# Optimization experiments

Measured on AMD Instinct MI355X. Metric: run time of the kernel, lower is better.

Reference implementation:

```python
import jax, jax.numpy as jnp
import numpy as np

B, C, H, W = 32, 1024, 48, 24
P = 3            # num_parts
IC = C // 8      # inter_channels for position attention
PH = H // P      # part height


def setup_inputs() -> dict:
    key = jax.random.key(0)
    ks = jax.random.split(key, 16)
    s = 0.02
    return {
        "x": jax.random.normal(ks[0], (B, C, H, W), jnp.float32),
        "modality": jax.random.randint(ks[1], (B,), 0, 2),
        # per-part 1x1 conv weights (stacked over parts)
        "Wq": jax.random.normal(ks[2], (P, IC, C), jnp.float32) * s,
        "bq": jnp.zeros((P, IC), jnp.float32),
        "Wk": jax.random.normal(ks[3], (P, IC, C), jnp.float32) * s,
        "bk": jnp.zeros((P, IC), jnp.float32),
        "Wv": jax.random.normal(ks[4], (P, C, C), jnp.float32) * s,
        "bv": jnp.zeros((P, C), jnp.float32),
        # gamma residual scales (torch inits to 0; random so output differs from x)
        "gamma_pa": jax.random.normal(ks[5], (P,), jnp.float32) * 0.1,
        "gamma_ca": jax.random.normal(ks[6], (P,), jnp.float32) * 0.1,
        # modality gate: Linear(1,64) -> ReLU -> Linear(64,P) -> Sigmoid
        "gW1": jax.random.normal(ks[7], (64, 1), jnp.float32) * 0.01,
        "gb1": jnp.zeros((64,), jnp.float32),
        "gW2": jax.random.normal(ks[8], (P, 64), jnp.float32) * 0.01,
        "gb2": jnp.zeros((P,), jnp.float32),
    }


def _part_dual_attn(part, Wq, bq, Wk, bk, Wv, bv, g_pa, g_ca):
    # part: [B, C, ph, W]
    b, c, ph, w = part.shape
    n = ph * w
    xf = part.reshape(b, c, n)  # [B,C,N]
    # --- Position attention (PAM) ---
    q = jnp.einsum('oc,bcn->bno', Wq, xf) + bq            # [B,N,IC]
    k = jnp.einsum('oc,bcn->bon', Wk, xf) + bk[:, None]   # [B,IC,N]
    attn = jax.nn.softmax(jnp.einsum('bno,bom->bnm', q, k), axis=-1)  # [B,N,N]
    v = jnp.einsum('oc,bcn->bon', Wv, xf) + bv[:, None]   # [B,C,N]
    pa = jnp.einsum('bcn,bmn->bcm', v, attn).reshape(part.shape)
    pa = g_pa * pa + part
    # --- Channel attention (CAM) with max-shifted softmax ---
    e = jnp.einsum('bcn,bdn->bcd', xf, xf)                # [B,C,C]
    e = jnp.max(e, axis=-1, keepdims=True) - e
    ca_attn = jax.nn.softmax(e, axis=-1)
    ca = jnp.einsum('bcd,bdn->bcn', ca_attn, xf).reshape(part.shape)
    ca = g_ca * ca + part
    return pa + ca


def reference(x, modality, Wq, bq, Wk, bk, Wv, bv, gamma_pa, gamma_ca, gW1, gb1, gW2, gb2):
    b = x.shape[0]
    # modality gate -> per-sample per-part blend weights [B,P]
    m = modality.astype(jnp.float32)[:, None]
    h = jax.nn.relu(m @ gW1.T + gb1)
    w_gate = jax.nn.sigmoid(h @ gW2.T + gb2)              # [B,P]
    # split into P horizontal parts: [P,B,C,ph,W]
    parts = x.reshape(b, C, P, PH, W).transpose(2, 0, 1, 3, 4)
    part_outs = jax.vmap(_part_dual_attn)(parts, Wq, bq, Wk, bk, Wv, bv, gamma_pa, gamma_ca)
    wp = w_gate.T[:, :, None, None, None]                 # [P,B,1,1,1]
    blended = parts * (1.0 - wp) + part_outs * wp         # [P,B,C,ph,W]
    return blended.transpose(1, 2, 0, 3, 4).reshape(b, C, H, W)
```

## Files before the change

### kernel.cpp

```cpp
#include <hip/hip_runtime.h>
#include <hip/hip_bf16.h>
#include <cstdint>

constexpr int kB  = 32;
constexpr int kC  = 1024;
constexpr int kH  = 48;
constexpr int kW  = 24;
constexpr int kP  = 3;
constexpr int kPH = 16;
constexpr int kN  = kPH * kW;
constexpr int kHW = kH * kW;
constexpr int64_t kCHW = (int64_t)kC * kHW;

typedef __attribute__((ext_vector_type(8))) short short8b;
typedef __attribute__((ext_vector_type(4))) float f32x4;

__device__ __forceinline__ void gl_lds16(const void* g, void* l) {
    __builtin_amdgcn_global_load_lds(
        (const __attribute__((address_space(1))) void*)g,
        (__attribute__((address_space(3))) void*)l, 16, 0, 0);
}

__device__ __forceinline__ void swz_block(int& bx, int& by, int& bz) {
    const int gx = gridDim.x, gy = gridDim.y, gz = gridDim.z;
    if ((gz & 7) == 0) {
        const int tpp = gx * gy;
        const int L   = (blockIdx.z * gy + blockIdx.y) * gx + blockIdx.x;
        const int xcd = L & 7;
        const int idx = L >> 3;
        const int ppx = gz >> 3;
        const int pairL = idx / tpp;
        const int tile  = idx - pairL * tpp;
        bz = xcd * ppx + pairL;
        by = tile / gx;
        bx = tile - by * gx;
    } else {
        bx = blockIdx.x; by = blockIdx.y; bz = blockIdx.z;
    }
}

#define WAIT8()       asm volatile("s_waitcnt vmcnt(8)" ::: "memory")
#define WAIT4()       asm volatile("s_waitcnt vmcnt(4)" ::: "memory")
#define WAIT0()       asm volatile("s_waitcnt vmcnt(0)" ::: "memory")
#define RAW_BARRIER() asm volatile("s_barrier" ::: "memory")
#define SFENCE()      __builtin_amdgcn_sched_barrier(0)

__global__ void gate_kernel(const int* __restrict__ modality,
                            const float* __restrict__ gW1, const float* __restrict__ gb1,
                            const float* __restrict__ gW2, const float* __restrict__ gb2,
                            const float* __restrict__ gpa, const float* __restrict__ gca,
                            const float* __restrict__ bq, const float* __restrict__ bk,
                            float* __restrict__ wg, float* __restrict__ cpa,
                            float* __restrict__ cca, float* __restrict__ bqk)
{
    const int t = threadIdx.x;
    if (t < 768) {
        const int p = t >> 8, o = t & 255;
        bqk[t] = (o < 128) ? bq[p * 128 + o] : bk[p * 128 + (o - 128)];
    }
    if (t < kB * kP) {
        const int b = t / kP, p = t % kP;
        const float m = (float)modality[b];
        float acc = gb2[p];
        #pragma unroll
        for (int j = 0; j < 64; ++j) {
            float h = fmaxf(fmaf(m, gW1[j], gb1[j]), 0.0f);
            acc = fmaf(gW2[p * 64 + j], h, acc);
        }
        const float w = 1.0f / (1.0f + __expf(-acc));
        wg[t]  = w;
        cpa[t] = w * gpa[p];
        cca[t] = w * gca[p];
    }
}

__global__ __launch_bounds__(256)
void wcast_kernel(const float* __restrict__ Wq, const float* __restrict__ Wk,
                  const float* __restrict__ Wv,
                  __hip_bfloat16* __restrict__ Wqkb, __hip_bfloat16* __restrict__ Wvb)
{
    const int64_t i = (int64_t)blockIdx.x * 256 + threadIdx.x;
    if (i < 196608) {
        const int64_t e = i * 4;
        const int p = (int)(e / 262144);
        const int rem = (int)(e % 262144);
        const int o = rem / 1024, c = rem % 1024;
        const float* s = (o < 128) ? (Wq + (int64_t)p * 131072 + (int64_t)o * 1024 + c)
                                   : (Wk + (int64_t)p * 131072 + (int64_t)(o - 128) * 1024 + c);
        float4 v = *(const float4*)s;
        __hip_bfloat16* d = Wqkb + e;
        d[0] = __float2bfloat16(v.x); d[1] = __float2bfloat16(v.y);
        d[2] = __float2bfloat16(v.z); d[3] = __float2bfloat16(v.w);
    } else if (i < 196608 + 786432) {
        const int64_t e = (i - 196608) * 4;
        float4 v = *(const float4*)(Wv + e);
        __hip_bfloat16* d = Wvb + e;
        d[0] = __float2bfloat16(v.x); d[1] = __float2bfloat16(v.y);
        d[2] = __float2bfloat16(v.z); d[3] = __float2bfloat16(v.w);
    }
}

__global__ void zeroz_kernel(float* __restrict__ Z)
{
    Z[(int64_t)blockIdx.x * 1024 + threadIdx.x] = 0.0f;
}

__global__ __launch_bounds__(256)
void cast_tr_kernel(const float* __restrict__ x,
                    __hip_bfloat16* __restrict__ xfb,
                    __hip_bfloat16* __restrict__ xfT)
{
    int bx, by, bz;
    swz_block(bx, by, bz);
    const int j = bz;
    const int bb = j / kP, pp = j % kP;
    const float* src = x + (int64_t)bb * kCHW + pp * kN;
    const int c0 = bx * 32, n0 = by * 32;
    __shared__ float tile[32][33];
    const int tx = threadIdx.x & 31, ty = threadIdx.x >> 5;
    #pragma unroll
    for (int r = 0; r < 4; ++r) {
        const int cl = ty * 4 + r;
        const int c = c0 + cl;
        float v = src[(int64_t)c * kHW + n0 + tx];
        xfb[(int64_t)j * 393216 + (int64_t)c * kN + n0 + tx] = __float2bfloat16(v);
        tile[tx][cl] = v;
    }
    __syncthreads();
    #pragma unroll
    for (int r = 0; r < 4; ++r) {
        const int nl = ty * 4 + r;
        xfT[(int64_t)j * 393216 + (int64_t)(n0 + nl) * kC + c0 + tx] =
            __float2bfloat16(tile[nl][tx]);
    }
}

template<int BIAS>
__global__ __launch_bounds__(256, 2)
void mm_kernel(const __hip_bfloat16* __restrict__ A0, int64_t aSB, int64_t aSP, int lda,
               const __hip_bfloat16* __restrict__ B0, int64_t bSB, int64_t bSP, int ldb,
               __hip_bfloat16* __restrict__ C0, int64_t cSB, int64_t cSP, int ldc,
               const float* __restrict__ bias0, int biasSP, int K)
{
    __shared__ char lds[65536];

    int bx, by, bz;
    swz_block(bx, by, bz);
    const int j = bz, bb = j / kP, pp = j % kP;
    const char* Ab = (const char*)(A0 + (int64_t)bb * aSB + (int64_t)pp * aSP);
    const char* Bb = (const char*)(B0 + (int64_t)bb * bSB + (int64_t)pp * bSP);
    const int m0 = bx * 128, n0 = by * 128;
    const int t = threadIdx.x, lane = t & 63, wv = t >> 6;
    const int wm = (wv & 1) * 64, wn = (wv >> 1) * 64;
    const size_t ldab = (size_t)lda * 2, ldbb = (size_t)ldb * 2;

    const int rr   = wv * 8 + (lane >> 3);
    const int gsrc = ((lane & 7) ^ (lane >> 3)) * 16;
    const int lrow = (wv * 8 + (lane >> 3)) * 128 + (lane & 7) * 16;

    auto STAGE = [&](int buf, int k0) {
        const char* Asrc = Ab + (size_t)(m0 + rr) * ldab + (size_t)k0 * 2 + gsrc;
        const char* Bsrc = Bb + (size_t)(n0 + rr) * ldbb + (size_t)k0 * 2 + gsrc;
        char* As = lds + buf * 32768;
        char* Bs = As + 16384;
        #pragma unroll
        for (int i = 0; i < 4; ++i) {
            gl_lds16(Asrc + (size_t)i * 32 * ldab, As + i * 4096 + lrow);
            gl_lds16(Bsrc + (size_t)i * 32 * ldbb, Bs + i * 4096 + lrow);
        }
    };

    f32x4 acc[4][4];
    #pragma unroll
    for (int a = 0; a < 4; ++a)
        #pragma unroll
        for (int b = 0; b < 4; ++b) acc[a][b] = (f32x4){0.f, 0.f, 0.f, 0.f};

    const int nk = K >> 6;
    STAGE(0, 0);
    int cur = 0;
    for (int k = 0; k < nk; ++k) {
        if (k + 1 < nk) { STAGE(cur ^ 1, (k + 1) << 6); WAIT8(); }
        else            { WAIT0(); }
        SFENCE();
        RAW_BARRIER();
        const char* As = lds + cur * 32768;
        const char* Bs = As + 16384;
        #pragma unroll
        for (int kk = 0; kk < 2; ++kk) {
            const int gpos = ((kk * 4 + (lane >> 4)) ^ (lane & 7)) * 16;
            short8b af[4], bf[4];
            #pragma unroll
            for (int f = 0; f < 4; ++f) {
                af[f] = *(const short8b*)(As + (wm + f * 16 + (lane & 15)) * 128 + gpos);
                bf[f] = *(const short8b*)(Bs + (wn + f * 16 + (lane & 15)) * 128 + gpos);
            }
            #pragma unroll
            for (int fm = 0; fm < 4; ++fm)
                #pragma unroll
                for (int fn = 0; fn < 4; ++fn)
                    acc[fm][fn] = __builtin_amdgcn_mfma_f32_16x16x32_bf16(
                        af[fm], bf[fn], acc[fm][fn], 0, 0, 0);
        }
        RAW_BARRIER();
        cur ^= 1;
    }

    __hip_bfloat16* Cm = C0 + (int64_t)bb * cSB + (int64_t)pp * cSP;
    #pragma unroll
    for (int fn = 0; fn < 4; ++fn) {
        const int col = n0 + wn + fn * 16 + (lane & 15);
        const float cb = (BIAS == 2) ? bias0[pp * biasSP + col] : 0.0f;
        #pragma unroll
        for (int fm = 0; fm < 4; ++fm)
            #pragma unroll
            for (int jr = 0; jr < 4; ++jr) {
                const int row = m0 + wm + fm * 16 + (lane >> 4) * 4 + jr;
                Cm[(int64_t)row * ldc + col] = __float2bfloat16(acc[fm][fn][jr] + cb);
            }
    }
}

__global__ __launch_bounds__(256, 2)
void ecam_kernel(const __hip_bfloat16* __restrict__ xfb,
                 __hip_bfloat16* __restrict__ eb,
                 float* __restrict__ Z)
{
    __shared__ char lds[65536];

    int bx, by, bz;
    swz_block(bx, by, bz);
    const int j = bz;
    int bi = 0;
    while ((bi + 1) * (bi + 2) / 2 <= bx) ++bi;
    const int bj = bx - bi * (bi + 1) / 2;
    const char* Ab = (const char*)(xfb + (int64_t)j * 393216);
    const int m0 = bi * 128, n0 = bj * 128;
    const int t = threadIdx.x, lane = t & 63, wv = t >> 6;
    const int wm = (wv & 1) * 64, wn = (wv >> 1) * 64;
    constexpr size_t ldab = 768;

    const int rr   = wv * 8 + (lane >> 3);
    const int gsrc = ((lane & 7) ^ (lane >> 3)) * 16;
    const int lrow = (wv * 8 + (lane >> 3)) * 128 + (lane & 7) * 16;

    auto STAGE = [&](int buf, int k0) {
        const char* Asrc = Ab + (size_t)(m0 + rr) * ldab + (size_t)k0 * 2 + gsrc;
        const char* Bsrc = Ab + (size_t)(n0 + rr) * ldab + (size_t)k0 * 2 + gsrc;
        char* As = lds + buf * 32768;
        char* Bs = As + 16384;
        #pragma unroll
        for (int i = 0; i < 4; ++i) {
            gl_lds16(Asrc + (size_t)i * 32 * ldab, As + i * 4096 + lrow);
            gl_lds16(Bsrc + (size_t)i * 32 * ldab, Bs + i * 4096 + lrow);
        }
    };

    f32x4 acc[4][4];
    #pragma unroll
    for (int a = 0; a < 4; ++a)
        #pragma unroll
        for (int b = 0; b < 4; ++b) acc[a][b] = (f32x4){0.f, 0.f, 0.f, 0.f};

    STAGE(0, 0);
    int cur = 0;
    for (int k = 0; k < 6; ++k) {
        if (k + 1 < 6) { STAGE(cur ^ 1, (k + 1) << 6); WAIT8(); }
        else           { WAIT0(); }
        SFENCE();
        RAW_BARRIER();
        const char* As = lds + cur * 32768;
        const char* Bs = As + 16384;
        #pragma unroll
        for (int kk = 0; kk < 2; ++kk) {
            const int gpos = ((kk * 4 + (lane >> 4)) ^ (lane & 7)) * 16;
            short8b af[4], bf[4];
            #pragma unroll
            for (int f = 0; f < 4; ++f) {
                af[f] = *(const short8b*)(As + (wm + f * 16 + (lane & 15)) * 128 + gpos);
                bf[f] = *(const short8b*)(Bs + (wn + f * 16 + (lane & 15)) * 128 + gpos);
            }
            #pragma unroll
            for (int fm = 0; fm < 4; ++fm)
                #pragma unroll
                for (int fn = 0; fn < 4; ++fn)
                    acc[fm][fn] = __builtin_amdgcn_mfma_f32_16x16x32_bf16(
                        af[fm], bf[fn], acc[fm][fn], 0, 0, 0);
        }
        RAW_BARRIER();
        cur ^= 1;
    }

    #pragma unroll
    for (int fm = 0; fm < 4; ++fm)
        #pragma unroll
        for (int fn = 0; fn < 4; ++fn)
            #pragma unroll
            for (int jr = 0; jr < 4; ++jr)
                acc[fm][fn][jr] = __expf(-60.f - acc[fm][fn][jr]);

    __hip_bfloat16* Cm = eb + (int64_t)j * 1048576;
    float* Zp = Z + (int64_t)j * 1024;

    #pragma unroll
    for (int fm = 0; fm < 4; ++fm)
        #pragma unroll
        for (int jr = 0; jr < 4; ++jr) {
            const int row = m0 + wm + fm * 16 + (lane >> 4) * 4 + jr;
            float v = 0.f;
            #pragma unroll
            for (int fn = 0; fn < 4; ++fn) {
                const int col = n0 + wn + fn * 16 + (lane & 15);
                Cm[(int64_t)row * 1024 + col] = __float2bfloat16(acc[fm][fn][jr]);
                v += acc[fm][fn][jr];
            }
            v += __shfl_xor(v, 1);
            v += __shfl_xor(v, 2);
            v += __shfl_xor(v, 4);
            v += __shfl_xor(v, 8);
            if ((lane & 15) == 0) atomicAdd(Zp + row, v);
        }

    if (bi != bj) {
        #pragma unroll
        for (int fn = 0; fn < 4; ++fn) {
            const int col = n0 + wn + fn * 16 + (lane & 15);
            float v2 = 0.f;
            #pragma unroll
            for (int fm = 0; fm < 4; ++fm) {
                const int row0 = m0 + wm + fm * 16 + (lane >> 4) * 4;
                __hip_bfloat16 h0 = __float2bfloat16(acc[fm][fn][0]);
                __hip_bfloat16 h1 = __float2bfloat16(acc[fm][fn][1]);
                __hip_bfloat16 h2 = __float2bfloat16(acc[fm][fn][2]);
                __hip_bfloat16 h3 = __float2bfloat16(acc[fm][fn][3]);
                ushort4 w4;
                w4.x = *(ushort*)&h0; w4.y = *(ushort*)&h1;
                w4.z = *(ushort*)&h2; w4.w = *(ushort*)&h3;
                *(ushort4*)((ushort*)Cm + (int64_t)col * 1024 + row0) = w4;
                v2 += (acc[fm][fn][0] + acc[fm][fn][1]) +
                      (acc[fm][fn][2] + acc[fm][fn][3]);
            }
            v2 += __shfl_xor(v2, 16);
            v2 += __shfl_xor(v2, 32);
            if ((lane >> 4) == 0) atomicAdd(Zp + col, v2);
        }
    }
}

__global__ __launch_bounds__(256, 3)
void ep_cam_kernel(const __hip_bfloat16* __restrict__ Wvb,
                   const __hip_bfloat16* __restrict__ yTb,
                   const __hip_bfloat16* __restrict__ eb,
                   const __hip_bfloat16* __restrict__ xfT,
                   const float* __restrict__ Z,
                   const float* __restrict__ x,
                   float* __restrict__ out,
                   const float* __restrict__ wg,
                   const float* __restrict__ cpa,
                   const float* __restrict__ cca,
                   const float* __restrict__ bv)
{
    __shared__ char lds[49152];

    int bx, by, bz;
    swz_block(bx, by, bz);
    const int j = bz, bb = j / kP, pp = j % kP;
    const int m0 = bx * 128, n0 = by * 128;
    const int t = threadIdx.x, lane = t & 63, wv = t >> 6;
    const int wm = (wv & 1) * 64, wn = (wv >> 1) * 64;

    const int rr4  = lane >> 2;
    const int gsrc = (((lane & 3) ^ ((lane >> 3) & 3)) * 16);
    const int ldst = lane * 16;

    const char* AbW = (const char*)(Wvb + (int64_t)pp * 1048576);
    const char* AbE = (const char*)(eb  + (int64_t)j  * 1048576);
    const char* BbY = (const char*)(yTb + (int64_t)j * 393216);
    const char* BbX = (const char*)(xfT + (int64_t)j * 393216);

    auto STAGE = [&](int buf, int g) {
        const char* A = (g < 32) ? AbE : AbW;
        const char* B = (g < 32) ? BbX : BbY;
        const size_t k0b = (size_t)(g & 31) * 64;
        const char* Asrc = A + (size_t)(m0 + wv * 32 + rr4) * 2048 + k0b + gsrc;
        const char* Bsrc = B + (size_t)(n0 + wv * 32 + rr4) * 2048 + k0b + gsrc;
        char* As = lds + buf * 16384;
        char* Bs = As + 8192;
        #pragma unroll
        for (int i = 0; i < 2; ++i) {
            gl_lds16(Asrc + (size_t)i * 16 * 2048, As + wv * 2048 + i * 1024 + ldst);
            gl_lds16(Bsrc + (size_t)i * 16 * 2048, Bs + wv * 2048 + i * 1024 + ldst);
        }
    };

    const float cfc = cca[j];
    const float* Zp = Z + (int64_t)j * 1024;
    float zsc[4][4];
    #pragma unroll
    for (int fm = 0; fm < 4; ++fm)
        #pragma unroll
        for (int jr = 0; jr < 4; ++jr) {
            const int row = m0 + wm + fm * 16 + (lane >> 4) * 4 + jr;
            zsc[fm][jr] = cfc / Zp[row];
        }

    f32x4 acc[4][4];
    #pragma unroll
    for (int a = 0; a < 4; ++a)
        #pragma unroll
        for (int b = 0; b < 4; ++b) acc[a][b] = (f32x4){0.f, 0.f, 0.f, 0.f};

    const int gpos = ((lane >> 4) ^ ((lane >> 1) & 3)) * 16;

    STAGE(0, 0);
    STAGE(1, 1);
    int cur = 0;
    for (int g = 0; g < 64; ++g) {
        if (g < 62) {
            int nb = cur + 2; if (nb >= 3) nb -= 3;
            STAGE(nb, g + 2);
            WAIT8();
        } else if (g == 62) { WAIT4(); }
        else                { WAIT0(); }
        SFENCE();
        RAW_BARRIER();
        if (g == 32) {
            #pragma unroll
            for (int fm = 0; fm < 4; ++fm)
                #pragma unroll
                for (int jr = 0; jr < 4; ++jr) {
                    const float zs = zsc[fm][jr];
                    #pragma unroll
                    for (int fn = 0; fn < 4; ++fn) acc[fm][fn][jr] *= zs;
                }
        }
        const char* As = lds + cur * 16384;
        const char* Bs = As + 8192;
        short8b af[4], bf[4];
        #pragma unroll
        for (int f = 0; f < 4; ++f) {
            af[f] = *(const short8b*)(As + (wm + f * 16 + (lane & 15)) * 64 + gpos);
            bf[f] = *(const short8b*)(Bs + (wn + f * 16 + (lane & 15)) * 64 + gpos);
        }
        #pragma unroll
        for (int fm = 0; fm < 4; ++fm)
            #pragma unroll
            for (int fn = 0; fn < 4; ++fn)
                acc[fm][fn] = __builtin_amdgcn_mfma_f32_16x16x32_bf16(
                    af[fm], bf[fn], acc[fm][fn], 0, 0, 0);
        RAW_BARRIER();
        if (++cur == 3) cur = 0;
    }

    const float gsc = 1.0f + wg[j];
    const float cfp = cpa[j];
    const float* Xm = x   + (int64_t)bb * kCHW + pp * kN;
    float*       Om = out + (int64_t)bb * kCHW + pp * kN;
    #pragma unroll
    for (int fm = 0; fm < 4; ++fm)
        #pragma unroll
        for (int jr = 0; jr < 4; ++jr) {
            const int row = m0 + wm + fm * 16 + (lane >> 4) * 4 + jr;
            const float rb = cfp * bv[pp * 1024 + row];
            #pragma unroll
            for (int fn = 0; fn < 4; ++fn) {
                const int col = n0 + wn + fn * 16 + (lane & 15);
                const int64_t off = (int64_t)row * kHW + col;
                Om[off] = fmaf(gsc, Xm[off], acc[fm][fn][jr] + rb);
            }
        }
}

__global__ __launch_bounds__(64) void sm_pam(__hip_bfloat16* __restrict__ buf,
                                             const float* __restrict__ scale,
                                             int chPairs)
{
    const int L = blockIdx.x;
    int pair, row;
    if ((chPairs & 7) == 0) {
        const int xcd = L & 7, idx = L >> 3;
        pair = xcd * (chPairs >> 3) + idx / kN;
        row  = idx % kN;
    } else { pair = L / kN; row = L % kN; }
    __hip_bfloat16* rp = buf + (int64_t)pair * (kN * kN) + (int64_t)row * kN;
    const int t = threadIdx.x;
    float v[6];
    float mx = -3.402823466e38f;
    #pragma unroll
    for (int r = 0; r < 6; ++r) {
        v[r] = __bfloat162float(rp[t + 64 * r]);
        mx = fmaxf(mx, v[r]);
    }
    #pragma unroll
    for (int off = 32; off > 0; off >>= 1) mx = fmaxf(mx, __shfl_xor(mx, off));
    float s = 0.0f;
    #pragma unroll
    for (int r = 0; r < 6; ++r) { v[r] = __expf(v[r] - mx); s += v[r]; }
    #pragma unroll
    for (int off = 32; off > 0; off >>= 1) s += __shfl_xor(s, off);
    const float inv = scale[pair] / s;
    #pragma unroll
    for (int r = 0; r < 6; ++r) rp[t + 64 * r] = __float2bfloat16(v[r] * inv);
}

extern "C" void kernel_launch(void* const* d_in, const int* in_sizes, int n_in,
                              void* d_out, int out_size, void* d_ws, size_t ws_size,
                              hipStream_t stream)
{
    const float* x   = (const float*)d_in[0];
    const int*   mod = (const int*)d_in[1];
    const float* Wq  = (const float*)d_in[2];
    const float* bq  = (const float*)d_in[3];
    const float* Wk  = (const float*)d_in[4];
    const float* bk  = (const float*)d_in[5];
    const float* Wv  = (const float*)d_in[6];
    const float* bv  = (const float*)d_in[7];
    const float* gpa = (const float*)d_in[8];
    const float* gca = (const float*)d_in[9];
    const float* gW1 = (const float*)d_in[10];
    const float* gb1 = (const float*)d_in[11];
    const float* gW2 = (const float*)d_in[12];
    const float* gb2 = (const float*)d_in[13];
    float* out = (float*)d_out;

    const int chList[6] = {96, 48, 24, 12, 6, 3};
    int CH = 3;
    for (int i = 0; i < 6; ++i) {
        size_t need = 7868544ull + (size_t)chList[i] * 4952064ull;
        if (need <= ws_size) { CH = chList[i]; break; }
    }
    const int NCHUNK = 96 / CH;

    char* ws = (char*)d_ws;
    __hip_bfloat16* Wqkb = (__hip_bfloat16*)(ws + 0);
    __hip_bfloat16* Wvb  = (__hip_bfloat16*)(ws + 1572864);
    float* bqk = (float*)(ws + 7864320);
    float* wg  = (float*)(ws + 7867392);
    float* cpa = (float*)(ws + 7867776);
    float* cca = (float*)(ws + 7868160);
    __hip_bfloat16* xfT   = (__hip_bfloat16*)(ws + 7868544);
    __hip_bfloat16* xfb   = xfT   + (int64_t)CH * 393216;
    __hip_bfloat16* qkT   = xfb   + (int64_t)CH * 393216;
    __hip_bfloat16* attnb = qkT   + (int64_t)CH * 98304;
    __hip_bfloat16* yTb   = attnb + (int64_t)CH * 147456;
    __hip_bfloat16* eb    = yTb   + (int64_t)CH * 393216;
    float*          Zbuf  = (float*)(eb + (int64_t)CH * 1048576);

    gate_kernel<<<1, 768, 0, stream>>>(mod, gW1, gb1, gW2, gb2, gpa, gca, bq, bk,
                                       wg, cpa, cca, bqk);
    wcast_kernel<<<3840, 256, 0, stream>>>(Wq, Wk, Wv, Wqkb, Wvb);

    for (int ch = 0; ch < NCHUNK; ++ch) {
        const int pair0 = ch * CH;
        const int b0 = pair0 / kP;
        const float* xc   = x   + (int64_t)b0 * kCHW;
        float*       outc = out + (int64_t)b0 * kCHW;

        cast_tr_kernel<<<dim3(32, 12, CH), 256, 0, stream>>>(xc, xfb, xfT);
        zeroz_kernel<<<CH, 1024, 0, stream>>>(Zbuf);

        mm_kernel<2><<<dim3(3, 2, CH), 256, 0, stream>>>(
            xfT, 3 * 393216, 393216, 1024,
            Wqkb, 0, 262144, 1024,
            qkT, 3 * 98304, 98304, 256,
            bqk, 256, 1024);
        mm_kernel<0><<<dim3(3, 3, CH), 256, 0, stream>>>(
            qkT, 3 * 98304, 98304, 256,
            qkT + 128, 3 * 98304, 98304, 256,
            attnb, 3 * 147456, 147456, 384,
            nullptr, 0, 128);
        sm_pam<<<CH * kN, 64, 0, stream>>>(attnb, cpa + pair0, CH);
        mm_kernel<0><<<dim3(3, 8, CH), 256, 0, stream>>>(
            attnb, 3 * 147456, 147456, 384,
            xfb, 3 * 393216, 393216, 384,
            yTb, 3 * 393216, 393216, 1024,
            nullptr, 0, 384);
        ecam_kernel<<<dim3(36, 1, CH), 256, 0, stream>>>(xfb, eb, Zbuf);
        ep_cam_kernel<<<dim3(8, 3, CH), 256, 0, stream>>>(
            Wvb, yTb, eb, xfT, Zbuf, xc, outc,
            wg + pair0, cpa + pair0, cca + pair0, bv);
    }
}
```

Before: 559.9 us.

## Enlarge ep_cam tile to 256x128 with 8 waves and interleaved LDS/MFMA phases

The CAM/value epilogue GEMM now uses 512-thread blocks, each computing a 256x128 output tile. K steps widen to 64 elements, so LDS reuse per global byte goes up and the main loop runs fewer iterations. The triple-buffered LDS grows to 144KB of dynamic shared memory with an 8-way XOR swizzle. Each K step is split into four barrier-separated sub-phases that interleave LDS fragment loads with MFMA bursts, and `s_setprio` raises wave priority during MFMA issue. In exchange, occupancy drops to one large block per CU, there are more barriers per step, and the kernel relies on a large dynamic LDS allocation being allowed.

Result: no change. 565.4 us (+1.0%).

```diff
diff --git a/kernel.cpp b/kernel.cpp
--- a/kernel.cpp
+++ b/kernel.cpp
@@ -40,8 +40,9 @@
 }
 
 #define WAIT8()       asm volatile("s_waitcnt vmcnt(8)" ::: "memory")
-#define WAIT4()       asm volatile("s_waitcnt vmcnt(4)" ::: "memory")
+#define WAIT6()       asm volatile("s_waitcnt vmcnt(6)" ::: "memory")
 #define WAIT0()       asm volatile("s_waitcnt vmcnt(0)" ::: "memory")
+#define LGKM0()       asm volatile("s_waitcnt lgkmcnt(0)" ::: "memory")
 #define RAW_BARRIER() asm volatile("s_barrier" ::: "memory")
 #define SFENCE()      __builtin_amdgcn_sched_barrier(0)
 
@@ -347,7 +348,7 @@
     }
 }
 
-__global__ __launch_bounds__(256, 3)
+__global__ __launch_bounds__(512, 2)
 void ep_cam_kernel(const __hip_bfloat16* __restrict__ Wvb,
                    const __hip_bfloat16* __restrict__ yTb,
                    const __hip_bfloat16* __restrict__ eb,
@@ -360,18 +361,18 @@
                    const float* __restrict__ cca,
                    const float* __restrict__ bv)
 {
-    __shared__ char lds[49152];
+    extern __shared__ char lds[];
 
     int bx, by, bz;
     swz_block(bx, by, bz);
     const int j = bz, bb = j / kP, pp = j % kP;
-    const int m0 = bx * 128, n0 = by * 128;
+    const int m0 = bx * 256, n0 = by * 128;
     const int t = threadIdx.x, lane = t & 63, wv = t >> 6;
-    const int wm = (wv & 1) * 64, wn = (wv >> 1) * 64;
-
-    const int rr4  = lane >> 2;
-    const int gsrc = (((lane & 3) ^ ((lane >> 3) & 3)) * 16);
-    const int ldst = lane * 16;
+    const int wm = (wv & 3) * 64, wn = (wv >> 2) * 64;
+
+    const int rr   = wv * 8 + (lane >> 3);
+    const int gsrc = ((lane & 7) ^ ((lane >> 3) & 7)) * 16;
+    const int ldst = wv * 1024 + lane * 16;
 
     const char* AbW = (const char*)(Wvb + (int64_t)pp * 1048576);
     const char* AbE = (const char*)(eb  + (int64_t)j  * 1048576);
@@ -379,18 +380,19 @@
     const char* BbX = (const char*)(xfT + (int64_t)j * 393216);
 
     auto STAGE = [&](int buf, int g) {
-        const char* A = (g < 32) ? AbE : AbW;
-        const char* B = (g < 32) ? BbX : BbY;
-        const size_t k0b = (size_t)(g & 31) * 64;
-        const char* Asrc = A + (size_t)(m0 + wv * 32 + rr4) * 2048 + k0b + gsrc;
-        const char* Bsrc = B + (size_t)(n0 + wv * 32 + rr4) * 2048 + k0b + gsrc;
-        char* As = lds + buf * 16384;
-        char* Bs = As + 8192;
-        #pragma unroll
-        for (int i = 0; i < 2; ++i) {
-            gl_lds16(Asrc + (size_t)i * 16 * 2048, As + wv * 2048 + i * 1024 + ldst);
-            gl_lds16(Bsrc + (size_t)i * 16 * 2048, Bs + wv * 2048 + i * 1024 + ldst);
-        }
+        const char* A = (g < 16) ? AbE : AbW;
+        const char* B = (g < 16) ? BbX : BbY;
+        const size_t k0b = (size_t)(g & 15) * 128;
+        const char* Asrc = A + (size_t)(m0 + rr) * 2048 + k0b + gsrc;
+        const char* Bsrc = B + (size_t)(n0 + rr) * 2048 + k0b + gsrc;
+        char* As = lds + (size_t)buf * 49152;
+        char* Bs = As + 32768;
+        #pragma unroll
+        for (int i = 0; i < 4; ++i)
+            gl_lds16(Asrc + (size_t)i * 64 * 2048, As + i * 8192 + ldst);
+        #pragma unroll
+        for (int i = 0; i < 2; ++i)
+            gl_lds16(Bsrc + (size_t)i * 64 * 2048, Bs + i * 8192 + ldst);
     };
 
     const float cfc = cca[j];
@@ -410,21 +412,33 @@
         #pragma unroll
         for (int b = 0; b < 4; ++b) acc[a][b] = (f32x4){0.f, 0.f, 0.f, 0.f};
 
-    const int gpos = ((lane >> 4) ^ ((lane >> 1) & 3)) * 16;
+    const int ro  = (lane & 15) * 128;
+    const int gp0 = (((lane >> 4)    ) ^ (lane & 7)) * 16;
+    const int gp1 = (((lane >> 4) + 4) ^ (lane & 7)) * 16;
+
+#define LDA_(FM, GP) (*(const short8b*)(As + (wm + (FM) * 16) * 128 + ro + (GP)))
+#define LDB_(FN, GP) (*(const short8b*)(Bs + (wn + (FN) * 16) * 128 + ro + (GP)))
+#define MM4(FM, AF)                                                              \
+    acc[FM][0] = __builtin_amdgcn_mfma_f32_16x16x32_bf16(AF, b0, acc[FM][0], 0, 0, 0); \
+    acc[FM][1] = __builtin_amdgcn_mfma_f32_16x16x32_bf16(AF, b1, acc[FM][1], 0, 0, 0); \
+    acc[FM][2] = __builtin_amdgcn_mfma_f32_16x16x32_bf16(AF, b2, acc[FM][2], 0, 0, 0); \
+    acc[FM][3] = __builtin_amdgcn_mfma_f32_16x16x32_bf16(AF, b3, acc[FM][3], 0, 0, 0);
 
     STAGE(0, 0);
     STAGE(1, 1);
+    WAIT6();
+    SFENCE();
+    RAW_BARRIER();
+
     int cur = 0;
-    for (int g = 0; g < 64; ++g) {
-        if (g < 62) {
-            int nb = cur + 2; if (nb >= 3) nb -= 3;
-            STAGE(nb, g + 2);
-            WAIT8();
-        } else if (g == 62) { WAIT4(); }
-        else                { WAIT0(); }
-        SFENCE();
-        RAW_BARRIER();
-        if (g == 32) {
+    #pragma unroll 1
+    for (int s = 0; s < 32; ++s) {
+        int nb = cur - 1; if (nb < 0) nb = 2;
+        const char* As = lds + (size_t)cur * 49152;
+        const char* Bs = As + 32768;
+        short8b a0, a1, a2, a3, b0, b1, b2, b3;
+
+        if (s == 16) {
             #pragma unroll
             for (int fm = 0; fm < 4; ++fm)
                 #pragma unroll
@@ -434,23 +448,49 @@
                     for (int fn = 0; fn < 4; ++fn) acc[fm][fn][jr] *= zs;
                 }
         }
-        const char* As = lds + cur * 16384;
-        const char* Bs = As + 8192;
-        short8b af[4], bf[4];
-        #pragma unroll
-        for (int f = 0; f < 4; ++f) {
-            af[f] = *(const short8b*)(As + (wm + f * 16 + (lane & 15)) * 64 + gpos);
-            bf[f] = *(const short8b*)(Bs + (wn + f * 16 + (lane & 15)) * 64 + gpos);
-        }
-        #pragma unroll
-        for (int fm = 0; fm < 4; ++fm)
-            #pragma unroll
-            for (int fn = 0; fn < 4; ++fn)
-                acc[fm][fn] = __builtin_amdgcn_mfma_f32_16x16x32_bf16(
-                    af[fm], bf[fn], acc[fm][fn], 0, 0, 0);
-        RAW_BARRIER();
-        if (++cur == 3) cur = 0;
-    }
+
+        a0 = LDA_(0, gp0); a1 = LDA_(1, gp0);
+        b0 = LDB_(0, gp0); b1 = LDB_(1, gp0); b2 = LDB_(2, gp0); b3 = LDB_(3, gp0);
+        if (s < 30) STAGE(nb, s + 2);
+        RAW_BARRIER();
+        LGKM0(); SFENCE();
+        __builtin_amdgcn_s_setprio(1);
+        MM4(0, a0); MM4(1, a1);
+        __builtin_amdgcn_s_setprio(0);
+        RAW_BARRIER();
+
+        a2 = LDA_(2, gp0); a3 = LDA_(3, gp0);
+        RAW_BARRIER();
+        LGKM0(); SFENCE();
+        __builtin_amdgcn_s_setprio(1);
+        MM4(2, a2); MM4(3, a3);
+        __builtin_amdgcn_s_setprio(0);
+        RAW_BARRIER();
+
+        a0 = LDA_(0, gp1); a1 = LDA_(1, gp1);
+        b0 = LDB_(0, gp1); b1 = LDB_(1, gp1); b2 = LDB_(2, gp1); b3 = LDB_(3, gp1);
+        RAW_BARRIER();
+        LGKM0(); SFENCE();
+        __builtin_amdgcn_s_setprio(1);
+        MM4(0, a0); MM4(1, a1);
+        __builtin_amdgcn_s_setprio(0);
+        RAW_BARRIER();
+
+        a2 = LDA_(2, gp1); a3 = LDA_(3, gp1);
+        RAW_BARRIER();
+        LGKM0(); SFENCE();
+        __builtin_amdgcn_s_setprio(1);
+        MM4(2, a2); MM4(3, a3);
+        __builtin_amdgcn_s_setprio(0);
+        if (s < 30) { WAIT6(); } else { WAIT0(); }
+        SFENCE();
+        RAW_BARRIER();
+
+        ++cur; if (cur == 3) cur = 0;
+    }
+#undef LDA_
+#undef LDB_
+#undef MM4
 
     const float gsc = 1.0f + wg[j];
     const float cfp = cpa[j];
@@ -576,7 +616,7 @@
             yTb, 3 * 393216, 393216, 1024,
             nullptr, 0, 384);
         ecam_kernel<<<dim3(36, 1, CH), 256, 0, stream>>>(xfb, eb, Zbuf);
-        ep_cam_kernel<<<dim3(8, 3, CH), 256, 0, stream>>>(
+        ep_cam_kernel<<<dim3(4, 3, CH), 512, 147456, stream>>>(
             Wvb, yTb, eb, xfT, Zbuf, xc, outc,
             wg + pair0, cpa + pair0, cca + pair0, bv);
     }
```

## Enlarge ep_cam tile to 512x128 with 8 waves and dynamic LDS

Applied to the files above, without the earlier changes.

Retiles the final fused CAM/value GEMM epilogue kernel from 128x128 tiles with 4 waves to 512x128 tiles with 8 waves. Each wave now computes a 128x64 sub-tile in two halves, and the triple-buffered LDS stages grow to 40 KB each (120 KB dynamic shared memory). The vmcnt waits are adjusted to match five loads per thread per stage. The aim is more reuse of the B operand and fewer redundant global loads. In exchange, occupancy drops to one block per CU, register pressure rises with 128 accumulator floats per thread, and the grid shrinks fourfold.

Result: slower. 605.3 us (+8.1%).

```diff
diff --git a/kernel.cpp b/kernel.cpp
--- a/kernel.cpp
+++ b/kernel.cpp
@@ -39,8 +39,9 @@
     }
 }
 
+#define WAIT10()      asm volatile("s_waitcnt vmcnt(10)" ::: "memory")
 #define WAIT8()       asm volatile("s_waitcnt vmcnt(8)" ::: "memory")
-#define WAIT4()       asm volatile("s_waitcnt vmcnt(4)" ::: "memory")
+#define WAIT5()       asm volatile("s_waitcnt vmcnt(5)" ::: "memory")
 #define WAIT0()       asm volatile("s_waitcnt vmcnt(0)" ::: "memory")
 #define RAW_BARRIER() asm volatile("s_barrier" ::: "memory")
 #define SFENCE()      __builtin_amdgcn_sched_barrier(0)
@@ -347,7 +348,7 @@
     }
 }
 
-__global__ __launch_bounds__(256, 3)
+__global__ __launch_bounds__(512, 1)
 void ep_cam_kernel(const __hip_bfloat16* __restrict__ Wvb,
                    const __hip_bfloat16* __restrict__ yTb,
                    const __hip_bfloat16* __restrict__ eb,
@@ -360,18 +361,18 @@
                    const float* __restrict__ cca,
                    const float* __restrict__ bv)
 {
-    __shared__ char lds[49152];
+    extern __shared__ char lds[];
 
     int bx, by, bz;
     swz_block(bx, by, bz);
     const int j = bz, bb = j / kP, pp = j % kP;
-    const int m0 = bx * 128, n0 = by * 128;
+    const int m0 = bx * 512, n0 = by * 128;
     const int t = threadIdx.x, lane = t & 63, wv = t >> 6;
-    const int wm = (wv & 1) * 64, wn = (wv >> 1) * 64;
-
-    const int rr4  = lane >> 2;
-    const int gsrc = (((lane & 3) ^ ((lane >> 3) & 3)) * 16);
-    const int ldst = lane * 16;
+    const int wm = (wv & 3) * 128, wn = (wv >> 2) * 64;
+
+    const int rr   = t >> 2;
+    const int gsrc = ((t & 3) ^ ((t >> 3) & 3)) * 16;
+    const int ldst = wv * 1024 + lane * 16;
 
     const char* AbW = (const char*)(Wvb + (int64_t)pp * 1048576);
     const char* AbE = (const char*)(eb  + (int64_t)j  * 1048576);
@@ -382,31 +383,30 @@
         const char* A = (g < 32) ? AbE : AbW;
         const char* B = (g < 32) ? BbX : BbY;
         const size_t k0b = (size_t)(g & 31) * 64;
-        const char* Asrc = A + (size_t)(m0 + wv * 32 + rr4) * 2048 + k0b + gsrc;
-        const char* Bsrc = B + (size_t)(n0 + wv * 32 + rr4) * 2048 + k0b + gsrc;
-        char* As = lds + buf * 16384;
-        char* Bs = As + 8192;
-        #pragma unroll
-        for (int i = 0; i < 2; ++i) {
-            gl_lds16(Asrc + (size_t)i * 16 * 2048, As + wv * 2048 + i * 1024 + ldst);
-            gl_lds16(Bsrc + (size_t)i * 16 * 2048, Bs + wv * 2048 + i * 1024 + ldst);
-        }
+        const char* Asrc = A + (size_t)(m0 + rr) * 2048 + k0b + gsrc;
+        const char* Bsrc = B + (size_t)(n0 + rr) * 2048 + k0b + gsrc;
+        char* As = lds + (size_t)buf * 40960;
+        char* Bs = As + 32768;
+        #pragma unroll
+        for (int i = 0; i < 4; ++i)
+            gl_lds16(Asrc + (size_t)i * 128 * 2048, As + i * 8192 + ldst);
+        gl_lds16(Bsrc, Bs + ldst);
     };
 
     const float cfc = cca[j];
     const float* Zp = Z + (int64_t)j * 1024;
-    float zsc[4][4];
-    #pragma unroll
-    for (int fm = 0; fm < 4; ++fm)
+    f32x4 zsc[8];
+    #pragma unroll
+    for (int fm = 0; fm < 8; ++fm)
         #pragma unroll
         for (int jr = 0; jr < 4; ++jr) {
             const int row = m0 + wm + fm * 16 + (lane >> 4) * 4 + jr;
             zsc[fm][jr] = cfc / Zp[row];
         }
 
-    f32x4 acc[4][4];
-    #pragma unroll
-    for (int a = 0; a < 4; ++a)
+    f32x4 acc[8][4];
+    #pragma unroll
+    for (int a = 0; a < 8; ++a)
         #pragma unroll
         for (int b = 0; b < 4; ++b) acc[a][b] = (f32x4){0.f, 0.f, 0.f, 0.f};
 
@@ -415,18 +415,19 @@
     STAGE(0, 0);
     STAGE(1, 1);
     int cur = 0;
+    #pragma unroll 1
     for (int g = 0; g < 64; ++g) {
         if (g < 62) {
             int nb = cur + 2; if (nb >= 3) nb -= 3;
             STAGE(nb, g + 2);
-            WAIT8();
-        } else if (g == 62) { WAIT4(); }
+            WAIT10();
+        } else if (g == 62) { WAIT5(); }
         else                { WAIT0(); }
         SFENCE();
         RAW_BARRIER();
         if (g == 32) {
             #pragma unroll
-            for (int fm = 0; fm < 4; ++fm)
+            for (int fm = 0; fm < 8; ++fm)
                 #pragma unroll
                 for (int jr = 0; jr < 4; ++jr) {
                     const float zs = zsc[fm][jr];
@@ -434,20 +435,36 @@
                     for (int fn = 0; fn < 4; ++fn) acc[fm][fn][jr] *= zs;
                 }
         }
-        const char* As = lds + cur * 16384;
-        const char* Bs = As + 8192;
-        short8b af[4], bf[4];
-        #pragma unroll
-        for (int f = 0; f < 4; ++f) {
-            af[f] = *(const short8b*)(As + (wm + f * 16 + (lane & 15)) * 64 + gpos);
+        const char* As = lds + (size_t)cur * 40960;
+        const char* Bs = As + 32768;
+        short8b bf[4];
+        #pragma unroll
+        for (int f = 0; f < 4; ++f)
             bf[f] = *(const short8b*)(Bs + (wn + f * 16 + (lane & 15)) * 64 + gpos);
-        }
-        #pragma unroll
-        for (int fm = 0; fm < 4; ++fm)
-            #pragma unroll
-            for (int fn = 0; fn < 4; ++fn)
-                acc[fm][fn] = __builtin_amdgcn_mfma_f32_16x16x32_bf16(
-                    af[fm], bf[fn], acc[fm][fn], 0, 0, 0);
+        {
+            short8b af[4];
+            #pragma unroll
+            for (int f = 0; f < 4; ++f)
+                af[f] = *(const short8b*)(As + (wm + f * 16 + (lane & 15)) * 64 + gpos);
+            #pragma unroll
+            for (int fm = 0; fm < 4; ++fm)
+                #pragma unroll
+                for (int fn = 0; fn < 4; ++fn)
+                    acc[fm][fn] = __builtin_amdgcn_mfma_f32_16x16x32_bf16(
+                        af[fm], bf[fn], acc[fm][fn], 0, 0, 0);
+        }
+        {
+            short8b af[4];
+            #pragma unroll
+            for (int f = 0; f < 4; ++f)
+                af[f] = *(const short8b*)(As + (wm + (f + 4) * 16 + (lane & 15)) * 64 + gpos);
+            #pragma unroll
+            for (int fm = 0; fm < 4; ++fm)
+                #pragma unroll
+                for (int fn = 0; fn < 4; ++fn)
+                    acc[fm + 4][fn] = __builtin_amdgcn_mfma_f32_16x16x32_bf16(
+                        af[fm], bf[fn], acc[fm + 4][fn], 0, 0, 0);
+        }
         RAW_BARRIER();
         if (++cur == 3) cur = 0;
     }
@@ -457,7 +474,7 @@
     const float* Xm = x   + (int64_t)bb * kCHW + pp * kN;
     float*       Om = out + (int64_t)bb * kCHW + pp * kN;
     #pragma unroll
-    for (int fm = 0; fm < 4; ++fm)
+    for (int fm = 0; fm < 8; ++fm)
         #pragma unroll
         for (int jr = 0; jr < 4; ++jr) {
             const int row = m0 + wm + fm * 16 + (lane >> 4) * 4 + jr;
@@ -576,7 +593,7 @@
             yTb, 3 * 393216, 393216, 1024,
             nullptr, 0, 384);
         ecam_kernel<<<dim3(36, 1, CH), 256, 0, stream>>>(xfb, eb, Zbuf);
-        ep_cam_kernel<<<dim3(8, 3, CH), 256, 0, stream>>>(
+        ep_cam_kernel<<<dim3(2, 3, CH), 512, 122880, stream>>>(
             Wvb, yTb, eb, xfT, Zbuf, xc, outc,
             wg + pair0, cpa + pair0, cca + pair0, bv);
     }
```
